# Performance work log

Hardware: AMD Instinct MI355X
Metric: run time of the kernel (lower is better)

The kernel has to match this reference:

```python
import math
import jax, jax.numpy as jnp
import numpy as np

B, T, D, NH = 4, 2048, 1024, 16
HS = D // NH
N_BUCKETS = 32
MAX_DIST = 128


def _relative_position_bucket(rp):
    # bidirectional T5 bucketing, n_buckets=32, max_distance=128
    nb = N_BUCKETS // 2  # 16
    buckets = (rp > 0).astype(jnp.int32) * nb
    rp = jnp.abs(rp)
    max_exact = nb // 2  # 8
    is_small = rp < max_exact
    me = max_exact - 1   # 7
    nbm = nb - 1         # 15
    rp_safe = jnp.maximum(rp, 1).astype(jnp.float32)
    rp_large = me + (jnp.log(rp_safe / me) / math.log(MAX_DIST / me) * (nbm - me)).astype(jnp.int32)
    rp_large = jnp.minimum(rp_large, nbm)
    buckets = buckets + jnp.where(is_small, rp, rp_large)
    return buckets


def compute_bias(rel_emb, qT, kT):
    ctx = jnp.arange(qT, dtype=jnp.int32)[:, None]
    mem = jnp.arange(kT, dtype=jnp.int32)[None, :]
    bucket = _relative_position_bucket(mem - ctx)  # [qT, kT]
    values = rel_emb[bucket]                        # [qT, kT, NH]
    return jnp.transpose(values, (2, 0, 1))[None]   # [1, NH, qT, kT]


def setup_inputs() -> dict:
    key = jax.random.key(0)
    ks = jax.random.split(key, 6)
    s = 0.02
    return {
        "queries": jax.random.normal(ks[0], (B, T, D), jnp.float32),
        "Wq": jax.random.normal(ks[1], (D, D), jnp.float32) * s,
        "Wk": jax.random.normal(ks[2], (D, D), jnp.float32) * s,
        "Wv": jax.random.normal(ks[3], (D, D), jnp.float32) * s,
        "Wo": jax.random.normal(ks[4], (D, D), jnp.float32) * s,
        "rel_emb": jax.random.normal(ks[5], (N_BUCKETS, NH), jnp.float32) * s,
    }


def reference(queries, Wq, Wk, Wv, Wo, rel_emb):
    b, t, d = queries.shape
    def split_heads(x):
        return jnp.transpose(x.reshape(b, t, NH, HS), (0, 2, 1, 3))  # [B, nh, T, hs]
    q = split_heads(queries @ Wq.T)
    k = split_heads(queries @ Wk.T)
    v = split_heads(queries @ Wv.T)
    att = jnp.einsum('bhqd,bhkd->bhqk', q, k) * (1.0 / math.sqrt(HS))
    att = att + compute_bias(rel_emb, t, t)
    att = jax.nn.softmax(att, axis=-1)
    o = jnp.einsum('bhqk,bhkd->bhqd', att, v)
    o = jnp.transpose(o, (0, 2, 1, 3)).reshape(b, t, d)
    return o @ Wo.T
```

## Files before the change

kernel.cpp:

```cpp
#include <hip/hip_runtime.h>

#define T_SEQ 2048
#define D_MODEL 1024
#define NHEADS 16
#define HSZ 64
#define BATCH 4

typedef __bf16 bf16x8 __attribute__((ext_vector_type(8)));
typedef __bf16 bf16x4 __attribute__((ext_vector_type(4)));
typedef short short4v __attribute__((ext_vector_type(4)));
typedef float f32x4 __attribute__((ext_vector_type(4)));

__device__ __forceinline__ unsigned short f2bf(float f) {
    unsigned int u = __builtin_bit_cast(unsigned int, f);
    u += 0x7fff + ((u >> 16) & 1);
    return (unsigned short)(u >> 16);
}

__device__ __forceinline__ unsigned int pk2bf(float a, float b) {
#if __has_builtin(__builtin_amdgcn_cvt_pk_bf16_f32)
    typedef __bf16 bf16x2_t __attribute__((ext_vector_type(2)));
    bf16x2_t v = __builtin_amdgcn_cvt_pk_bf16_f32(a, b);
    return __builtin_bit_cast(unsigned int, v);
#else
    return (unsigned int)f2bf(a) | ((unsigned int)f2bf(b) << 16);
#endif
}

__device__ __forceinline__ float fexp2(float x) {
#if __has_builtin(__builtin_amdgcn_exp2f)
    return __builtin_amdgcn_exp2f(x);
#else
    return __builtin_exp2f(x);
#endif
}

__device__ __forceinline__ f32x4 mfma16_bf16(short4v a, short4v b, f32x4 c) {
#if __has_builtin(__builtin_amdgcn_mfma_f32_16x16x16_bf16)
    return __builtin_amdgcn_mfma_f32_16x16x16_bf16(
        __builtin_bit_cast(bf16x4, a), __builtin_bit_cast(bf16x4, b), c, 0, 0, 0);
#elif __has_builtin(__builtin_amdgcn_mfma_f32_16x16x16bf16_1k)
    return __builtin_amdgcn_mfma_f32_16x16x16bf16_1k(a, b, c, 0, 0, 0);
#else
    f32x4 d;
    asm volatile("v_mfma_f32_16x16x16_bf16 %0, %1, %2, %3"
                 : "=v"(d) : "v"(a), "v"(b), "v"(c));
    return d;
#endif
}

__device__ __forceinline__ void gld_lds16(const void* g, void* lds) {
    __builtin_amdgcn_global_load_lds(
        (const __attribute__((address_space(1))) unsigned int*)g,
        (__attribute__((address_space(3))) unsigned int*)lds, 16, 0, 0);
}

__device__ __forceinline__ bf16x8 ld8(const unsigned short* p) {
    return *(const bf16x8*)p;
}

__global__ void cast_x(const float* __restrict__ src, unsigned short* __restrict__ dst, int n4) {
    int i = blockIdx.x * blockDim.x + threadIdx.x;
    if (i >= n4) return;
    float4 v = ((const float4*)src)[i];
    ushort4 o;
    o.x = f2bf(v.x); o.y = f2bf(v.y); o.z = f2bf(v.z); o.w = f2bf(v.w);
    ((ushort4*)dst)[i] = o;
}

__global__ void cast_w(const float* __restrict__ w0, const float* __restrict__ w1,
                       const float* __restrict__ w2, const float* __restrict__ w3,
                       unsigned short* __restrict__ dst) {
    const float* srcs[4] = {w0, w1, w2, w3};
    int wsel = blockIdx.y;
    const float4* src = (const float4*)srcs[wsel];
    int i = blockIdx.x * blockDim.x + threadIdx.x;
    float4 v = src[i];
    ushort4 o;
    o.x = f2bf(v.x); o.y = f2bf(v.y); o.z = f2bf(v.z); o.w = f2bf(v.w);
    ((ushort4*)(dst + (size_t)wsel * 1048576))[i] = o;
}

__global__ void bias_table(const float* __restrict__ rel_emb, float* __restrict__ bias_tab) {
    int idx = blockIdx.x * blockDim.x + threadIdx.x;
    if (idx >= NHEADS * 4095) return;
    int h = idx / 4095;
    int rp = (idx % 4095) - 2047;
    int bucket = rp > 0 ? 16 : 0;
    int arp = rp < 0 ? -rp : rp;
    if (arp < 8) {
        bucket += arp;
    } else {
        float f = logf((float)arp / 7.0f) * (8.0f / logf(128.0f / 7.0f));
        int rl = 7 + (int)f;
        bucket += rl < 15 ? rl : 15;
    }
    bias_tab[idx] = rel_emb[bucket * NHEADS + h] * 1.4426950408889634f;
}

template<int MODE>
__global__ __launch_bounds__(256, 2) void gemm_bt(
    const unsigned short* __restrict__ A,
    const unsigned short* __restrict__ Bw,
    void* __restrict__ out)
{
    constexpr int K = 1024;
    __shared__ unsigned short As[128 * 64];
    __shared__ unsigned short Bs[128 * 64];

    const int tid  = threadIdx.x;
    const int wave = tid >> 6;
    const int lane = tid & 63;
    const int quad = lane >> 4;
    const int l16  = lane & 15;
    const int wm   = wave >> 1;
    const int wn   = wave & 1;
    const int bn   = blockIdx.x;
    const int bm   = blockIdx.y;

    const int r_in = lane >> 3;
    const int lc   = (lane & 7) ^ r_in;

    f32x4 acc[4][4];
    #pragma unroll
    for (int m = 0; m < 4; ++m)
        #pragma unroll
        for (int n = 0; n < 4; ++n)
            acc[m][n] = f32x4{0.f, 0.f, 0.f, 0.f};

    const long a_row0 = (long)bm * 128;
    const long b_row0 = (long)bn * 128;

    for (int kt = 0; kt < K / 64; ++kt) {
        __syncthreads();
        const int k0 = kt * 64 + lc * 8;
        #pragma unroll
        for (int c = 0; c < 4; ++c) {
            int cc = wave * 4 + c;
            int r  = cc * 8 + r_in;
            gld_lds16(A  + (a_row0 + r) * K + k0, &As[cc * 512]);
            gld_lds16(Bw + (b_row0 + r) * K + k0, &Bs[cc * 512]);
        }
        __syncthreads();

        bf16x8 af[4][2], bf[4][2];
        #pragma unroll
        for (int m = 0; m < 4; ++m)
            #pragma unroll
            for (int ks = 0; ks < 2; ++ks) {
                int r  = wm * 64 + m * 16 + l16;
                int pc = (ks * 4 + quad) ^ (r & 7);
                af[m][ks] = ld8(&As[r * 64 + pc * 8]);
            }
        #pragma unroll
        for (int n = 0; n < 4; ++n)
            #pragma unroll
            for (int ks = 0; ks < 2; ++ks) {
                int r  = wn * 64 + n * 16 + l16;
                int pc = (ks * 4 + quad) ^ (r & 7);
                bf[n][ks] = ld8(&Bs[r * 64 + pc * 8]);
            }
        #pragma unroll
        for (int ks = 0; ks < 2; ++ks)
            #pragma unroll
            for (int m = 0; m < 4; ++m)
                #pragma unroll
                for (int n = 0; n < 4; ++n)
                    acc[m][n] = __builtin_amdgcn_mfma_f32_16x16x32_bf16(
                        af[m][ks], bf[n][ks], acc[m][n], 0, 0, 0);
    }

    const int which = (MODE == 4) ? (bn >> 3) : 0;
    #pragma unroll
    for (int m = 0; m < 4; ++m) {
        int row = bm * 128 + wm * 64 + m * 16 + quad * 4;
        #pragma unroll
        for (int n = 0; n < 4; ++n) {
            int col = bn * 128 + wn * 64 + n * 16 + l16;
            if (MODE == 3) {
                float* O = (float*)out;
                #pragma unroll
                for (int r = 0; r < 4; ++r)
                    O[(long)(row + r) * 1024 + col] = acc[m][n][r];
            } else {
                int cl = col & 1023;
                int h = cl >> 6, hs = cl & 63;
                int b = row >> 11, t = row & 2047;
                unsigned short* O = (unsigned short*)out + (size_t)which * 8388608;
                if (which == 2) {
                    ushort4 pk;
                    pk.x = f2bf(acc[m][n][0]); pk.y = f2bf(acc[m][n][1]);
                    pk.z = f2bf(acc[m][n][2]); pk.w = f2bf(acc[m][n][3]);
                    *(ushort4*)&O[(long)((b * 16 + h) * 64 + hs) * 2048 + t] = pk;
                } else {
                    #pragma unroll
                    for (int r = 0; r < 4; ++r) {
                        float v = acc[m][n][r];
                        if (which == 0) v *= 0.125f * 1.4426950408889634f;
                        O[(long)((b * 16 + h) * 2048 + (t + r)) * 64 + hs] = f2bf(v);
                    }
                }
            }
        }
    }
}

__global__ __launch_bounds__(256, 2) void attn(
    const unsigned short* __restrict__ Q,
    const unsigned short* __restrict__ Kb,
    const unsigned short* __restrict__ Vt,
    const float* __restrict__ bias_tab,
    unsigned short* __restrict__ AO)
{
    __shared__ __align__(16) char smem[41984];
    unsigned short* KsB = (unsigned short*)smem;
    unsigned short* VsB = (unsigned short*)(smem + 16384);
    float*          Bb  = (float*)(smem + 32768);

    const int tid  = threadIdx.x;
    const int wave = tid >> 6;
    const int lane = tid & 63;
    const int quad = lane >> 4;
    const int l16  = lane & 15;

    const int bh = blockIdx.y;
    const int b  = bh >> 4, h = bh & 15;
    const int q0 = blockIdx.x * 256;

    const unsigned short* Qg = Q  + (long)bh * T_SEQ * HSZ;
    const unsigned short* Kg = Kb + (long)bh * T_SEQ * HSZ;
    const unsigned short* Vg = Vt + (long)bh * HSZ * T_SEQ;

    const int r_in = lane >> 3;
    const int lc   = (lane & 7) ^ r_in;

    {
        #pragma unroll
        for (int c = 0; c < 2; ++c) {
            int cc = wave * 2 + c;
            int r  = cc * 8 + r_in;
            gld_lds16(Kg + (long)r * 64 + lc * 8, &KsB[cc * 512]);
            gld_lds16(Vg + (long)r * T_SEQ + lc * 8, &VsB[cc * 512]);
        }
    }

    {
        const float* bt = bias_tab + h * 4095 + (1792 - q0);
        for (int i = tid; i < 2303; i += 256) Bb[i] = bt[i];
    }

    bf16x8 qf[4][2];
    #pragma unroll
    for (int nt = 0; nt < 4; ++nt)
        #pragma unroll
        for (int ks = 0; ks < 2; ++ks) {
            int t = q0 + wave * 64 + nt * 16 + l16;
            qf[nt][ks] = ld8(&Qg[(long)t * 64 + ks * 32 + quad * 8]);
        }

    f32x4 o[4][4];
    float li[4];
    #pragma unroll
    for (int nq = 0; nq < 4; ++nq)
        #pragma unroll
        for (int nh = 0; nh < 4; ++nh) o[nq][nh] = f32x4{0.f, 0.f, 0.f, 0.f};
    #pragma unroll
    for (int nq = 0; nq < 4; ++nq) li[nq] = 0.0f;

    float cneg, cpos;
    {
        const float* bt = bias_tab + h * 4095;
        cneg = bt[0];
        cpos = bt[4094];
    }

    for (int kt = 0; kt < T_SEQ / 64; ++kt) {
        const int cur = kt & 1;
        __syncthreads();

        if (kt + 1 < T_SEQ / 64) {
            unsigned short* Kn = KsB + (cur ^ 1) * 4096;
            unsigned short* Vn = VsB + (cur ^ 1) * 4096;
            #pragma unroll
            for (int c = 0; c < 2; ++c) {
                int cc = wave * 2 + c;
                int r  = cc * 8 + r_in;
                gld_lds16(Kg + (long)((kt + 1) * 64 + r) * 64 + lc * 8, &Kn[cc * 512]);
                gld_lds16(Vg + (long)r * T_SEQ + (kt + 1) * 64 + lc * 8, &Vn[cc * 512]);
            }
        }

        const unsigned short* Ks = KsB + cur * 4096;
        const unsigned short* Vs = VsB + cur * 4096;

        const int lo = kt * 64 - q0 - 255;
        const int hi = kt * 64 + 63 - q0;
        const bool outband = (lo >= 128) || (hi <= -128);
        const float cb = (lo >= 128) ? cpos : cneg;
        const f32x4 cbv = {cb, cb, cb, cb};

        short4v pfrag[4][4];
        #pragma unroll
        for (int kc = 0; kc < 4; ++kc) {
            int rk = kc * 16 + l16;
            bf16x8 kf0 = ld8(&Ks[rk * 64 + ((quad)     ^ (rk & 7)) * 8]);
            bf16x8 kf1 = ld8(&Ks[rk * 64 + ((4 + quad) ^ (rk & 7)) * 8]);
            #pragma unroll
            for (int nq = 0; nq < 4; ++nq) {
                f32x4 c0;
                if (outband) {
                    c0 = cbv;
                } else {
                    int i0 = kt * 64 + kc * 16 + quad * 4
                           - wave * 64 - nq * 16 - l16 + 255;
                    c0 = f32x4{Bb[i0], Bb[i0 + 1], Bb[i0 + 2], Bb[i0 + 3]};
                }
                f32x4 s = __builtin_amdgcn_mfma_f32_16x16x32_bf16(kf0, qf[nq][0], c0, 0, 0, 0);
                s = __builtin_amdgcn_mfma_f32_16x16x32_bf16(kf1, qf[nq][1], s, 0, 0, 0);
                float p[4];
                #pragma unroll
                for (int r = 0; r < 4; ++r) p[r] = fexp2(s[r]);
                li[nq] += (p[0] + p[1]) + (p[2] + p[3]);
                uint2 pk = {pk2bf(p[0], p[1]), pk2bf(p[2], p[3])};
                pfrag[kc][nq] = __builtin_bit_cast(short4v, pk);
            }
        }

        #pragma unroll
        for (int kc = 0; kc < 4; ++kc) {
            short4v vf[4];
            #pragma unroll
            for (int nh = 0; nh < 4; ++nh) {
                int rv = nh * 16 + l16;
                int ch = (kc * 2 + (quad >> 1)) ^ (rv & 7);
                vf[nh] = *(const short4v*)&Vs[rv * 64 + ch * 8 + (quad & 1) * 4];
            }
            #pragma unroll
            for (int nq = 0; nq < 4; ++nq)
                #pragma unroll
                for (int nh = 0; nh < 4; ++nh)
                    o[nq][nh] = mfma16_bf16(pfrag[kc][nq], vf[nh], o[nq][nh]);
        }
    }

    #pragma unroll
    for (int nq = 0; nq < 4; ++nq) {
        li[nq] += __shfl_xor(li[nq], 16);
        li[nq] += __shfl_xor(li[nq], 32);
    }
    float inv[4];
    #pragma unroll
    for (int nq = 0; nq < 4; ++nq) inv[nq] = 1.0f / li[nq];

    #pragma unroll
    for (int nq = 0; nq < 4; ++nq) {
        float iv[4];
        #pragma unroll
        for (int r = 0; r < 4; ++r) iv[r] = __shfl(inv[nq], quad * 4 + r);
        int qrow = q0 + wave * 64 + nq * 16 + quad * 4;
        #pragma unroll
        for (int r = 0; r < 4; ++r)
            #pragma unroll
            for (int nh = 0; nh < 4; ++nh)
                AO[(long)(b * T_SEQ + qrow + r) * D_MODEL + h * 64 + nh * 16 + l16] =
                    f2bf(o[nq][nh][r] * iv[r]);
    }
}

extern "C" void kernel_launch(void* const* d_in, const int* in_sizes, int n_in,
                              void* d_out, int out_size, void* d_ws, size_t ws_size,
                              hipStream_t stream) {
    const float* x   = (const float*)d_in[0];
    const float* wq  = (const float*)d_in[1];
    const float* wk  = (const float*)d_in[2];
    const float* wv  = (const float*)d_in[3];
    const float* wo  = (const float*)d_in[4];
    const float* rel = (const float*)d_in[5];

    char* ws = (char*)d_ws;
    unsigned short* Xbf = (unsigned short*)(ws);
    unsigned short* Wbf = (unsigned short*)(ws + (16l << 20));
    unsigned short* Qb  = (unsigned short*)(ws + (24l << 20));
    float*          btb = (float*)(ws + (72l << 20));

    cast_x<<<8192, 256, 0, stream>>>(x, Xbf, 2097152);
    cast_w<<<dim3(1024, 4), 256, 0, stream>>>(wq, wk, wv, wo, Wbf);
    bias_table<<<256, 256, 0, stream>>>(rel, btb);

    gemm_bt<4><<<dim3(24, 64), 256, 0, stream>>>(Xbf, Wbf, Qb);

    unsigned short* Kbf = Qb + 8388608;
    unsigned short* Vtb = Qb + 16777216;
    unsigned short* AO  = Xbf;
    attn<<<dim3(8, 64), 256, 0, stream>>>(Qb, Kbf, Vtb, btb, AO);

    gemm_bt<3><<<dim3(8, 64), 256, 0, stream>>>(AO, Wbf + 3 * 1048576, d_out);
}
```

Before: 294.9 us.

## Fuse prep kernels and stage Q/K epilogue through LDS for coalesced stores

Merges the three preprocessing kernels (input cast, weight cast, bias table) into one launch to cut launch overhead. The QKV GEMM epilogue for Q and K now writes bf16 results into per-wave LDS tiles, then copies 64x64 head tiles out with 16-byte coalesced stores instead of scattered 2-byte stores. This adds an LDS round trip and a larger shared buffer, which may affect occupancy.

```diff
diff --git a/kernel.cpp b/kernel.cpp
--- a/kernel.cpp
+++ b/kernel.cpp
@@ -59,43 +59,45 @@
     return *(const bf16x8*)p;
 }
 
-__global__ void cast_x(const float* __restrict__ src, unsigned short* __restrict__ dst, int n4) {
-    int i = blockIdx.x * blockDim.x + threadIdx.x;
-    if (i >= n4) return;
-    float4 v = ((const float4*)src)[i];
-    ushort4 o;
-    o.x = f2bf(v.x); o.y = f2bf(v.y); o.z = f2bf(v.z); o.w = f2bf(v.w);
-    ((ushort4*)dst)[i] = o;
-}
-
-__global__ void cast_w(const float* __restrict__ w0, const float* __restrict__ w1,
-                       const float* __restrict__ w2, const float* __restrict__ w3,
-                       unsigned short* __restrict__ dst) {
-    const float* srcs[4] = {w0, w1, w2, w3};
-    int wsel = blockIdx.y;
-    const float4* src = (const float4*)srcs[wsel];
-    int i = blockIdx.x * blockDim.x + threadIdx.x;
-    float4 v = src[i];
-    ushort4 o;
-    o.x = f2bf(v.x); o.y = f2bf(v.y); o.z = f2bf(v.z); o.w = f2bf(v.w);
-    ((ushort4*)(dst + (size_t)wsel * 1048576))[i] = o;
-}
-
-__global__ void bias_table(const float* __restrict__ rel_emb, float* __restrict__ bias_tab) {
-    int idx = blockIdx.x * blockDim.x + threadIdx.x;
-    if (idx >= NHEADS * 4095) return;
-    int h = idx / 4095;
-    int rp = (idx % 4095) - 2047;
-    int bucket = rp > 0 ? 16 : 0;
-    int arp = rp < 0 ? -rp : rp;
-    if (arp < 8) {
-        bucket += arp;
+__global__ void prep(const float* __restrict__ x,
+                     const float* __restrict__ w0, const float* __restrict__ w1,
+                     const float* __restrict__ w2, const float* __restrict__ w3,
+                     const float* __restrict__ rel,
+                     unsigned short* __restrict__ Xbf,
+                     unsigned short* __restrict__ Wbf,
+                     float* __restrict__ bias_tab) {
+    int bid = blockIdx.x;
+    int tid = threadIdx.x;
+    if (bid < 8192) {
+        int i = bid * 256 + tid;
+        float4 v = ((const float4*)x)[i];
+        ushort4 o;
+        o.x = f2bf(v.x); o.y = f2bf(v.y); o.z = f2bf(v.z); o.w = f2bf(v.w);
+        ((ushort4*)Xbf)[i] = o;
+    } else if (bid < 12288) {
+        int wsel = (bid - 8192) >> 10;
+        const float* srcs[4] = {w0, w1, w2, w3};
+        int i = ((bid - 8192) & 1023) * 256 + tid;
+        float4 v = ((const float4*)srcs[wsel])[i];
+        ushort4 o;
+        o.x = f2bf(v.x); o.y = f2bf(v.y); o.z = f2bf(v.z); o.w = f2bf(v.w);
+        ((ushort4*)(Wbf + (size_t)wsel * 1048576))[i] = o;
     } else {
-        float f = logf((float)arp / 7.0f) * (8.0f / logf(128.0f / 7.0f));
-        int rl = 7 + (int)f;
-        bucket += rl < 15 ? rl : 15;
-    }
-    bias_tab[idx] = rel_emb[bucket * NHEADS + h] * 1.4426950408889634f;
+        int idx = (bid - 12288) * 256 + tid;
+        if (idx >= NHEADS * 4095) return;
+        int h = idx / 4095;
+        int rp = (idx % 4095) - 2047;
+        int bucket = rp > 0 ? 16 : 0;
+        int arp = rp < 0 ? -rp : rp;
+        if (arp < 8) {
+            bucket += arp;
+        } else {
+            float f = logf((float)arp / 7.0f) * (8.0f / logf(128.0f / 7.0f));
+            int rl = 7 + (int)f;
+            bucket += rl < 15 ? rl : 15;
+        }
+        bias_tab[idx] = rel[bucket * NHEADS + h] * 1.4426950408889634f;
+    }
 }
 
 template<int MODE>
@@ -105,8 +107,9 @@
     void* __restrict__ out)
 {
     constexpr int K = 1024;
-    __shared__ unsigned short As[128 * 64];
-    __shared__ unsigned short Bs[128 * 64];
+    __shared__ __align__(16) char smem[36864];
+    unsigned short* As = (unsigned short*)smem;
+    unsigned short* Bs = (unsigned short*)(smem + 16384);
 
     const int tid  = threadIdx.x;
     const int wave = tid >> 6;
@@ -171,36 +174,61 @@
     }
 
     const int which = (MODE == 4) ? (bn >> 3) : 0;
-    #pragma unroll
-    for (int m = 0; m < 4; ++m) {
-        int row = bm * 128 + wm * 64 + m * 16 + quad * 4;
-        #pragma unroll
-        for (int n = 0; n < 4; ++n) {
-            int col = bn * 128 + wn * 64 + n * 16 + l16;
-            if (MODE == 3) {
-                float* O = (float*)out;
+    if (MODE == 3) {
+        float* O = (float*)out;
+        #pragma unroll
+        for (int m = 0; m < 4; ++m) {
+            int row = bm * 128 + wm * 64 + m * 16 + quad * 4;
+            #pragma unroll
+            for (int n = 0; n < 4; ++n) {
+                int col = bn * 128 + wn * 64 + n * 16 + l16;
                 #pragma unroll
                 for (int r = 0; r < 4; ++r)
                     O[(long)(row + r) * 1024 + col] = acc[m][n][r];
-            } else {
-                int cl = col & 1023;
+            }
+        }
+    } else if (which == 2) {
+        unsigned short* O = (unsigned short*)out + (size_t)2 * 8388608;
+        #pragma unroll
+        for (int m = 0; m < 4; ++m) {
+            int row = bm * 128 + wm * 64 + m * 16 + quad * 4;
+            int b = row >> 11, t = row & 2047;
+            #pragma unroll
+            for (int n = 0; n < 4; ++n) {
+                int cl = (bn * 128 + wn * 64 + n * 16 + l16) & 1023;
                 int h = cl >> 6, hs = cl & 63;
-                int b = row >> 11, t = row & 2047;
-                unsigned short* O = (unsigned short*)out + (size_t)which * 8388608;
-                if (which == 2) {
-                    ushort4 pk;
-                    pk.x = f2bf(acc[m][n][0]); pk.y = f2bf(acc[m][n][1]);
-                    pk.z = f2bf(acc[m][n][2]); pk.w = f2bf(acc[m][n][3]);
-                    *(ushort4*)&O[(long)((b * 16 + h) * 64 + hs) * 2048 + t] = pk;
-                } else {
-                    #pragma unroll
-                    for (int r = 0; r < 4; ++r) {
-                        float v = acc[m][n][r];
-                        if (which == 0) v *= 0.125f * 1.4426950408889634f;
-                        O[(long)((b * 16 + h) * 2048 + (t + r)) * 64 + hs] = f2bf(v);
-                    }
-                }
-            }
+                ushort4 pk;
+                pk.x = f2bf(acc[m][n][0]); pk.y = f2bf(acc[m][n][1]);
+                pk.z = f2bf(acc[m][n][2]); pk.w = f2bf(acc[m][n][3]);
+                *(ushort4*)&O[(long)((b * 16 + h) * 64 + hs) * 2048 + t] = pk;
+            }
+        }
+    } else {
+        __syncthreads();
+        unsigned short* Ew = (unsigned short*)smem + wave * 4608;
+        const float qs = (which == 0) ? 0.125f * 1.4426950408889634f : 1.0f;
+        #pragma unroll
+        for (int m = 0; m < 4; ++m)
+            #pragma unroll
+            for (int n = 0; n < 4; ++n)
+                #pragma unroll
+                for (int r = 0; r < 4; ++r)
+                    Ew[(m * 16 + quad * 4 + r) * 72 + n * 16 + l16] =
+                        f2bf(acc[m][n][r] * qs);
+        asm volatile("s_waitcnt lgkmcnt(0)" ::: "memory");
+
+        const int cl0 = (bn * 128 + wn * 64) & 1023;
+        const int h   = cl0 >> 6;
+        const int gr0 = bm * 128 + wm * 64;
+        const int b   = gr0 >> 11, t0 = gr0 & 2047;
+        unsigned short* O = (unsigned short*)out + (size_t)which * 8388608
+                          + ((size_t)(b * 16 + h) * 2048 + t0) * 64;
+        #pragma unroll
+        for (int rr = 0; rr < 8; ++rr) {
+            int row   = rr * 8 + (lane >> 3);
+            int chunk = lane & 7;
+            uint4 v = *(const uint4*)&Ew[row * 72 + chunk * 8];
+            *(uint4*)&O[(size_t)row * 64 + chunk * 8] = v;
         }
     }
 }
@@ -383,9 +411,7 @@
     unsigned short* Qb  = (unsigned short*)(ws + (24l << 20));
     float*          btb = (float*)(ws + (72l << 20));
 
-    cast_x<<<8192, 256, 0, stream>>>(x, Xbf, 2097152);
-    cast_w<<<dim3(1024, 4), 256, 0, stream>>>(wq, wk, wv, wo, Wbf);
-    bias_table<<<256, 256, 0, stream>>>(rel, btb);
+    prep<<<12544, 256, 0, stream>>>(x, wq, wk, wv, wo, rel, Xbf, Wbf, btb);
 
     gemm_bt<4><<<dim3(24, 64), 256, 0, stream>>>(Xbf, Wbf, Qb);
 
```

After: 268.0 us. 9.1% less time.
